# Performance work log

Measured on AMD Instinct MI355X. Metric: run time of the kernel, lower is better.

The kernel has to match this reference:

```python
import jax, jax.numpy as jnp
import numpy as np

N_NODES = 50000
N_EDGES = 800000
IN_CH = 128
HID = 256


def gcn_layer(x, src, dst, W, b, n_nodes):
    # x: [N, F_in] -> h: [N, F_out]
    h = x @ W
    # add self loops (PyG GCNConv default)
    loop = jnp.arange(n_nodes, dtype=src.dtype)
    src_f = jnp.concatenate([src, loop])
    dst_f = jnp.concatenate([dst, loop])
    # symmetric normalization: deg^{-1/2}[src] * deg^{-1/2}[dst]
    deg = jax.ops.segment_sum(jnp.ones_like(dst_f, dtype=h.dtype), dst_f, num_segments=n_nodes)
    dinv = jnp.where(deg > 0, jax.lax.rsqrt(deg), 0.0)
    norm = dinv[src_f] * dinv[dst_f]  # [E+N]
    msg = h[src_f] * norm[:, None]    # [E+N, F_out] gather
    out = jax.ops.segment_sum(msg, dst_f, num_segments=n_nodes)  # scatter-add
    return out + b


def setup_inputs() -> dict:
    key = jax.random.key(0)
    k1, k2, k3, k4 = jax.random.split(key, 4)
    x = jax.random.normal(k1, (N_NODES, IN_CH), dtype=jnp.float32)
    edge_index = jax.random.randint(k2, (2, N_EDGES), 0, N_NODES, dtype=jnp.int64)
    W1 = jax.random.normal(k3, (IN_CH, HID), dtype=jnp.float32) * (1.0 / np.sqrt(IN_CH))
    b1 = jnp.zeros((HID,), dtype=jnp.float32)
    W2 = jax.random.normal(k4, (HID, HID), dtype=jnp.float32) * (1.0 / np.sqrt(HID))
    b2 = jnp.zeros((HID,), dtype=jnp.float32)
    return {"x": x, "edge_index": edge_index, "W1": W1, "b1": b1, "W2": W2, "b2": b2}


def reference(x, edge_index, W1, b1, W2, b2):
    src, dst = edge_index[0], edge_index[1]
    h = gcn_layer(x, src, dst, W1, b1, N_NODES)
    h = jax.nn.relu(h)
    # dropout in eval mode (training=False) is identity
    out = gcn_layer(h, src, dst, W2, b2, N_NODES)
    return out
```

## Files before the change

kernel.cpp:

```cpp
#include <hip/hip_runtime.h>

constexpr int N = 50000;
constexpr int E = 800000;
constexpr int NPAD = 50048;
constexpr int NB = (N + 255) / 256;

typedef _Float16 half8 __attribute__((ext_vector_type(8)));
typedef _Float16 half4v __attribute__((ext_vector_type(4)));
typedef float float4v __attribute__((ext_vector_type(4)));

__global__ __launch_bounds__(256) void deg_kernel(const int* __restrict__ dst,
                                                  int* __restrict__ degI) {
    int e = blockIdx.x * 256 + threadIdx.x;
    if (e < E) atomicAdd(&degI[dst[e]], 1);
}

__global__ __launch_bounds__(256) void dinv_kernel(const int* __restrict__ degI,
                                                   float* __restrict__ dinv) {
    int v = blockIdx.x * 256 + threadIdx.x;
    if (v < N) dinv[v] = rsqrtf((float)degI[v] + 1.0f);
}

__global__ __launch_bounds__(256) void scan1_kernel(const int* __restrict__ degI,
                                                    int* __restrict__ incl,
                                                    int* __restrict__ blockSums) {
    __shared__ int s[256];
    int t = threadIdx.x;
    int i = blockIdx.x * 256 + t;
    int d = (i < N) ? degI[i] : 0;
    s[t] = d;
    __syncthreads();
    for (int off = 1; off < 256; off <<= 1) {
        int v = s[t];
        int u = (t >= off) ? s[t - off] : 0;
        __syncthreads();
        s[t] = v + u;
        __syncthreads();
    }
    if (i < N) incl[i] = s[t];
    if (t == 255) blockSums[blockIdx.x] = s[255];
}

__global__ __launch_bounds__(256) void scan2_kernel(int* __restrict__ blockSums) {
    __shared__ int s[256];
    int t = threadIdx.x;
    int v = (t < NB) ? blockSums[t] : 0;
    s[t] = v;
    __syncthreads();
    for (int off = 1; off < 256; off <<= 1) {
        int a = s[t];
        int u = (t >= off) ? s[t - off] : 0;
        __syncthreads();
        s[t] = a + u;
        __syncthreads();
    }
    if (t < NB) blockSums[t] = s[t] - v;
}

__global__ __launch_bounds__(256) void scan3_kernel(const int* __restrict__ degI,
                                                    const int* __restrict__ incl,
                                                    const int* __restrict__ blockSums,
                                                    int* __restrict__ rowptr,
                                                    int* __restrict__ cursor) {
    int i = blockIdx.x * 256 + threadIdx.x;
    if (i < N) {
        int e = blockSums[blockIdx.x] + incl[i] - degI[i];
        rowptr[i] = e;
        cursor[i] = e;
    }
    if (i == 0) rowptr[N] = E;
}

__global__ __launch_bounds__(256) void fill_kernel(const int* __restrict__ src,
                                                   const int* __restrict__ dst,
                                                   int* __restrict__ cursor,
                                                   int* __restrict__ eidx) {
    int e = blockIdx.x * 256 + threadIdx.x;
    if (e >= E) return;
    int d = dst[e];
    int pos = atomicAdd(&cursor[d], 1);
    eidx[pos] = src[e];
}

template <int K>
__global__ __launch_bounds__(256) void wt_kernel(const float* __restrict__ W,
                                                 _Float16* __restrict__ Wt) {
    int idx = blockIdx.x * 256 + threadIdx.x;
    int k = idx & (K - 1);
    int n = idx >> (K == 128 ? 7 : 8);
    Wt[idx] = (_Float16)W[(size_t)k * 256 + n];
}

__global__ __launch_bounds__(256) void prescale_kernel(const float4* __restrict__ x,
                                                       const float* __restrict__ dinv,
                                                       half4v* __restrict__ px) {
    int idx = blockIdx.x * 256 + threadIdx.x;
    if (idx >= N * 32) return;
    float dv = dinv[idx >> 5];
    float4 t = x[idx];
    half4v o;
    o[0] = (_Float16)(t.x * dv);
    o[1] = (_Float16)(t.y * dv);
    o[2] = (_Float16)(t.z * dv);
    o[3] = (_Float16)(t.w * dv);
    px[idx] = o;
}

template <int C4>
__global__ __launch_bounds__(256) void aggregate_f16(
    const int* __restrict__ rowptr, const int* __restrict__ eidx,
    const half4v* __restrict__ f, const float* __restrict__ dinv,
    half4v* __restrict__ q) {
    int v = blockIdx.x * (256 / C4) + threadIdx.x / C4;
    if (v >= N) return;
    int lane = threadIdx.x % C4;
    int beg = rowptr[v];
    int end = rowptr[v + 1];

    half4v sv = f[(size_t)v * C4 + lane];
    float a0 = (float)sv[0], a1 = (float)sv[1], a2 = (float)sv[2], a3 = (float)sv[3];

    int i = beg;
    for (; i + 8 <= end; i += 8) {
        int e0 = eidx[i + 0], e1 = eidx[i + 1], e2 = eidx[i + 2], e3 = eidx[i + 3];
        int e4 = eidx[i + 4], e5 = eidx[i + 5], e6 = eidx[i + 6], e7 = eidx[i + 7];
        half4v t0 = f[(size_t)e0 * C4 + lane];
        half4v t1 = f[(size_t)e1 * C4 + lane];
        half4v t2 = f[(size_t)e2 * C4 + lane];
        half4v t3 = f[(size_t)e3 * C4 + lane];
        half4v t4 = f[(size_t)e4 * C4 + lane];
        half4v t5 = f[(size_t)e5 * C4 + lane];
        half4v t6 = f[(size_t)e6 * C4 + lane];
        half4v t7 = f[(size_t)e7 * C4 + lane];
        a0 += ((float)t0[0] + (float)t1[0]) + ((float)t2[0] + (float)t3[0]) +
              ((float)t4[0] + (float)t5[0]) + ((float)t6[0] + (float)t7[0]);
        a1 += ((float)t0[1] + (float)t1[1]) + ((float)t2[1] + (float)t3[1]) +
              ((float)t4[1] + (float)t5[1]) + ((float)t6[1] + (float)t7[1]);
        a2 += ((float)t0[2] + (float)t1[2]) + ((float)t2[2] + (float)t3[2]) +
              ((float)t4[2] + (float)t5[2]) + ((float)t6[2] + (float)t7[2]);
        a3 += ((float)t0[3] + (float)t1[3]) + ((float)t2[3] + (float)t3[3]) +
              ((float)t4[3] + (float)t5[3]) + ((float)t6[3] + (float)t7[3]);
    }
    for (; i + 2 <= end; i += 2) {
        int e0 = eidx[i], e1 = eidx[i + 1];
        half4v t0 = f[(size_t)e0 * C4 + lane];
        half4v t1 = f[(size_t)e1 * C4 + lane];
        a0 += (float)t0[0] + (float)t1[0];
        a1 += (float)t0[1] + (float)t1[1];
        a2 += (float)t0[2] + (float)t1[2];
        a3 += (float)t0[3] + (float)t1[3];
    }
    if (i < end) {
        half4v t0 = f[(size_t)eidx[i] * C4 + lane];
        a0 += (float)t0[0];
        a1 += (float)t0[1];
        a2 += (float)t0[2];
        a3 += (float)t0[3];
    }

    float dv = dinv[v];
    half4v o;
    o[0] = (_Float16)(a0 * dv);
    o[1] = (_Float16)(a1 * dv);
    o[2] = (_Float16)(a2 * dv);
    o[3] = (_Float16)(a3 * dv);
    q[(size_t)v * C4 + lane] = o;
}

template <int K, bool FUSE1>
__global__ __launch_bounds__(256) void gemm_mfma(
    const _Float16* __restrict__ A, const _Float16* __restrict__ Wt,
    const float* __restrict__ bias, const float* __restrict__ dinv,
    void* __restrict__ outp) {
    int wave = threadIdx.x >> 6;
    int lane = threadIdx.x & 63;
    int m = lane & 15;
    int quad = lane >> 4;
    int rbase = blockIdx.x * 64 + wave * 16;
    int cbase = blockIdx.y * 64;

    float4v acc[4] = {};

    const half8* Arow = (const half8*)(A + (size_t)(rbase + m) * K);
#pragma unroll
    for (int k0 = 0; k0 < K; k0 += 32) {
        half8 a = Arow[(k0 >> 3) + quad];
#pragma unroll
        for (int c = 0; c < 4; ++c) {
            const half8* Brow = (const half8*)(Wt + (size_t)(cbase + c * 16 + m) * K);
            half8 b = Brow[(k0 >> 3) + quad];
            acc[c] = __builtin_amdgcn_mfma_f32_16x16x32_f16(a, b, acc[c], 0, 0, 0);
        }
    }

#pragma unroll
    for (int c = 0; c < 4; ++c) {
        int col = cbase + c * 16 + m;
        float bcol = bias[col];
#pragma unroll
        for (int r = 0; r < 4; ++r) {
            int row = rbase + quad * 4 + r;
            if (row < N) {
                float val = acc[c][r] + bcol;
                if (FUSE1) {
                    val = fmaxf(val, 0.f) * dinv[row];
                    ((_Float16*)outp)[(size_t)row * 256 + col] = (_Float16)val;
                } else {
                    ((float*)outp)[(size_t)row * 256 + col] = val;
                }
            }
        }
    }
}

extern "C" void kernel_launch(void* const* d_in, const int* in_sizes, int n_in,
                              void* d_out, int out_size, void* d_ws, size_t ws_size,
                              hipStream_t stream) {
    const float* x  = (const float*)d_in[0];
    const int* edge = (const int*)d_in[1];
    const int* src  = edge;
    const int* dst  = edge + E;
    const float* W1 = (const float*)d_in[2];
    const float* b1 = (const float*)d_in[3];
    const float* W2 = (const float*)d_in[4];
    const float* b2 = (const float*)d_in[5];
    float* out = (float*)d_out;

    _Float16* bufA = (_Float16*)d_ws;
    _Float16* bufB = bufA + (size_t)NPAD * 256;
    float* dinv    = (float*)(bufB + (size_t)NPAD * 256);
    int* degI      = (int*)(dinv + N);
    int* rowptr    = degI + N;
    int* cursor    = rowptr + (N + 1);
    int* eidx      = cursor + N;
    _Float16* W1t  = (_Float16*)(eidx + E);
    _Float16* W2t  = W1t + 256 * 128;
    int* blockSums = (int*)(W2t + 256 * 256);

    hipMemsetAsync(degI, 0, N * sizeof(int), stream);
    deg_kernel<<<(E + 255) / 256, 256, 0, stream>>>(dst, degI);
    dinv_kernel<<<(N + 255) / 256, 256, 0, stream>>>(degI, dinv);
    scan1_kernel<<<NB, 256, 0, stream>>>(degI, cursor, blockSums);
    scan2_kernel<<<1, 256, 0, stream>>>(blockSums);
    scan3_kernel<<<NB, 256, 0, stream>>>(degI, cursor, blockSums, rowptr, cursor);
    fill_kernel<<<(E + 255) / 256, 256, 0, stream>>>(src, dst, cursor, eidx);

    wt_kernel<128><<<(256 * 128) / 256, 256, 0, stream>>>(W1, W1t);
    wt_kernel<256><<<(256 * 256) / 256, 256, 0, stream>>>(W2, W2t);

    prescale_kernel<<<(N * 32 + 255) / 256, 256, 0, stream>>>(
        (const float4*)x, dinv, (half4v*)bufA);
    aggregate_f16<32><<<(N + 7) / 8, 256, 0, stream>>>(
        rowptr, eidx, (const half4v*)bufA, dinv, (half4v*)bufB);
    gemm_mfma<128, true><<<dim3(NPAD / 64, 4), 256, 0, stream>>>(
        bufB, W1t, b1, dinv, bufA);

    aggregate_f16<64><<<(N + 3) / 4, 256, 0, stream>>>(
        rowptr, eidx, (const half4v*)bufA, dinv, (half4v*)bufB);
    gemm_mfma<256, false><<<dim3(NPAD / 64, 4), 256, 0, stream>>>(
        bufB, W2t, b2, dinv, out);
}
```

Baseline: 376.6 us.

## Keep A fragments in registers and stage weight tiles in LDS per column chunk

Each GEMM block now covers all 256 output columns: it loads its 16-row A fragments into registers once and loops over four 64-column chunks, copying each weight chunk into padded shared memory before the MFMA loop. This removes the fourfold re-read of A from the old column-split grid and replaces scattered global weight loads with LDS reads. In exchange the grid is four times smaller, register use grows (up to 8 half8 fragments for K=256), LDS use is up to about 33 KB per block, and barriers are added between chunks.

```diff
diff --git a/kernel.cpp b/kernel.cpp
--- a/kernel.cpp
+++ b/kernel.cpp
@@ -172,41 +172,63 @@
     const _Float16* __restrict__ A, const _Float16* __restrict__ Wt,
     const float* __restrict__ bias, const float* __restrict__ dinv,
     void* __restrict__ outp) {
-    int wave = threadIdx.x >> 6;
-    int lane = threadIdx.x & 63;
-    int m = lane & 15;
-    int quad = lane >> 4;
-    int rbase = blockIdx.x * 64 + wave * 16;
-    int cbase = blockIdx.y * 64;
-
-    float4v acc[4] = {};
-
-    const half8* Arow = (const half8*)(A + (size_t)(rbase + m) * K);
-#pragma unroll
-    for (int k0 = 0; k0 < K; k0 += 32) {
-        half8 a = Arow[(k0 >> 3) + quad];
+    constexpr int LSTR = K + 8;
+    __shared__ _Float16 Bs[64 * LSTR];
+
+    const int tid = threadIdx.x;
+    const int wave = tid >> 6;
+    const int lane = tid & 63;
+    const int m = lane & 15;
+    const int quad = lane >> 4;
+    const int rbase = blockIdx.x * 64 + wave * 16;
+    const int row = rbase + m;
+
+    half8 af[K / 32];
+    {
+        const half8* Arow = (const half8*)(A + (size_t)row * K);
+#pragma unroll
+        for (int i = 0; i < K / 32; ++i) af[i] = Arow[i * 4 + quad];
+    }
+
+    for (int cc = 0; cc < 4; ++cc) {
+        const int colbase = cc * 64;
+        if (cc) __syncthreads();
+        {
+            int col = tid >> 2;
+            int sub = tid & 3;
+            const half8* srcb = (const half8*)(Wt + (size_t)(colbase + col) * K);
+            half8* dstb = (half8*)&Bs[col * LSTR];
+#pragma unroll
+            for (int u = 0; u < K / 32; ++u) dstb[sub + u * 4] = srcb[sub + u * 4];
+        }
+        __syncthreads();
+
+        float4v acc[4] = {};
+#pragma unroll
+        for (int k0 = 0; k0 < K; k0 += 32) {
+            half8 a = af[k0 >> 5];
+#pragma unroll
+            for (int c = 0; c < 4; ++c) {
+                half8 b = *(const half8*)&Bs[(c * 16 + m) * LSTR + k0 + quad * 8];
+                acc[c] = __builtin_amdgcn_mfma_f32_16x16x32_f16(a, b, acc[c], 0, 0, 0);
+            }
+        }
+
 #pragma unroll
         for (int c = 0; c < 4; ++c) {
-            const half8* Brow = (const half8*)(Wt + (size_t)(cbase + c * 16 + m) * K);
-            half8 b = Brow[(k0 >> 3) + quad];
-            acc[c] = __builtin_amdgcn_mfma_f32_16x16x32_f16(a, b, acc[c], 0, 0, 0);
-        }
-    }
-
-#pragma unroll
-    for (int c = 0; c < 4; ++c) {
-        int col = cbase + c * 16 + m;
-        float bcol = bias[col];
-#pragma unroll
-        for (int r = 0; r < 4; ++r) {
-            int row = rbase + quad * 4 + r;
-            if (row < N) {
-                float val = acc[c][r] + bcol;
-                if (FUSE1) {
-                    val = fmaxf(val, 0.f) * dinv[row];
-                    ((_Float16*)outp)[(size_t)row * 256 + col] = (_Float16)val;
-                } else {
-                    ((float*)outp)[(size_t)row * 256 + col] = val;
+            int col = colbase + c * 16 + m;
+            float bcol = bias[col];
+#pragma unroll
+            for (int r = 0; r < 4; ++r) {
+                int orow = rbase + quad * 4 + r;
+                if (orow < N) {
+                    float val = acc[c][r] + bcol;
+                    if (FUSE1) {
+                        val = fmaxf(val, 0.f) * dinv[orow];
+                        ((_Float16*)outp)[(size_t)orow * 256 + col] = (_Float16)val;
+                    } else {
+                        ((float*)outp)[(size_t)orow * 256 + col] = val;
+                    }
                 }
             }
         }
@@ -252,11 +274,11 @@
         (const float4*)x, dinv, (half4v*)bufA);
     aggregate_f16<32><<<(N + 7) / 8, 256, 0, stream>>>(
         rowptr, eidx, (const half4v*)bufA, dinv, (half4v*)bufB);
-    gemm_mfma<128, true><<<dim3(NPAD / 64, 4), 256, 0, stream>>>(
+    gemm_mfma<128, true><<<NPAD / 64, 256, 0, stream>>>(
         bufB, W1t, b1, dinv, bufA);
 
     aggregate_f16<64><<<(N + 3) / 4, 256, 0, stream>>>(
         rowptr, eidx, (const half4v*)bufA, dinv, (half4v*)bufB);
-    gemm_mfma<256, false><<<dim3(NPAD / 64, 4), 256, 0, stream>>>(
+    gemm_mfma<256, false><<<NPAD / 64, 256, 0, stream>>>(
         bufB, W2t, b2, dinv, out);
 }
```

Measured after the change: 321.6 us. 14.6% less time.
